# Kernel optimization log

Hardware: AMD Instinct MI355X
Metric: run time of the kernel (lower is better)

The kernel has to match this reference:

```python
import jax, jax.numpy as jnp
import numpy as np

S_IN, S_OUT = 64, 128
NX, NS, CIN, COUT = 40000, 200000, 128, 64


def _unique_coords(key, n, S):
    lin = jax.random.permutation(key, S ** 3)[:n]
    return jnp.stack([lin // (S * S), (lin // S) % S, lin % S], axis=-1).astype(jnp.int32)


def setup_inputs() -> dict:
    key = jax.random.key(0)
    ks = jax.random.split(key, 8)
    cords = _unique_coords(ks[0], NX, S_IN)          # unique low-res coords
    skip_cords = _unique_coords(ks[1], NS, S_OUT)    # unique high-res coords
    x_feats = jax.random.normal(ks[2], (NX, CIN), jnp.float32)
    skip_feats = jax.random.normal(ks[3], (NS, COUT), jnp.float32)
    w_up = jax.random.normal(ks[4], (8, CIN, COUT), jnp.float32) * 0.05
    w1 = jax.random.normal(ks[5], (27, COUT, COUT), jnp.float32) * 0.05
    w2 = jax.random.normal(ks[6], (27, COUT, COUT), jnp.float32) * 0.05
    w3 = jax.random.normal(ks[7], (27, COUT, COUT), jnp.float32) * 0.05
    ones = jnp.ones((COUT,), jnp.float32)
    zeros = jnp.zeros((COUT,), jnp.float32)
    return dict(x_feats=x_feats, skip_feats=skip_feats, w_up=w_up, w1=w1, w2=w2, w3=w3,
                g1=ones, b1=zeros, g2=ones, b2=zeros, g3=ones, b3=zeros,
                cords=cords, skip_cords=skip_cords, spatial_size=64)


def _lin(c, S):
    return (c[..., 0] * S + c[..., 1]) * S + c[..., 2]


def _bn(f, g, b):
    # BatchNorm1d, batch stats (track_running_stats=False), eps=1e-4, biased var
    mu = f.mean(axis=0)
    var = f.var(axis=0)
    return (f - mu) * jax.lax.rsqrt(var + 1e-4) * g + b


def _lrelu(z, s):
    return jnp.where(z >= 0, z, s * z)


def reference(x_feats, skip_feats, w_up, w1, w2, w3, g1, b1, g2, b2, g3, b3,
              cords, skip_cords, spatial_size):
    S = 2 * int(spatial_size)  # output spatial size after upsample
    Cout = w_up.shape[-1]
    # --- upsample: each active voxel c emits a 2x2x2 block at 2c+o, weight W[1-o] ---
    offs8 = jnp.stack(jnp.meshgrid(*([jnp.arange(2)] * 3), indexing='ij'), -1).reshape(8, 3).astype(jnp.int32)
    out_cords = ((2 * cords)[:, None, :] + offs8[None, :, :]).reshape(-1, 3)        # [8N,3]
    feats = jnp.einsum('nc,ocd->nod', x_feats, w_up[::-1]).reshape(-1, Cout)         # [8N,C]
    M = feats.shape[0]
    lin_out = _lin(out_cords, S)
    # --- sparse_add: hash-match skip coords, add matched skip features ---
    table_s = jnp.full((S ** 3,), -1, jnp.int32).at[_lin(skip_cords, S)].set(
        jnp.arange(skip_cords.shape[0], dtype=jnp.int32))
    j = table_s[lin_out]
    feats = feats + jnp.where((j >= 0)[:, None], skip_feats[jnp.clip(j, 0)], 0.0)
    # --- neighbor table for 3x3x3 submanifold convs over the fixed active set ---
    table_o = jnp.full((S ** 3,), -1, jnp.int32).at[lin_out].set(jnp.arange(M, dtype=jnp.int32))
    offs27 = jnp.stack(jnp.meshgrid(*([jnp.arange(-1, 2)] * 3), indexing='ij'), -1).reshape(27, 3).astype(jnp.int32)
    nb = out_cords[None, :, :] + offs27[:, None, :]                                  # [27,M,3]
    valid = jnp.all((nb >= 0) & (nb < S), axis=-1)
    lin_nb = jnp.where(valid, _lin(nb, S), 0)
    nbr = jnp.where(valid, table_o[lin_nb], -1)                                      # [27,M]

    def subconv(f, W):
        acc = jnp.zeros((M, W.shape[-1]), f.dtype)
        for k in range(27):  # fixed small kernel loop
            idx = nbr[k]
            m = (idx >= 0).astype(f.dtype)[:, None]
            acc = acc + (f[jnp.clip(idx, 0)] * m) @ W[k]
        return acc

    x1 = _lrelu(_bn(subconv(feats, w1), g1, b1), 0.05)
    x2 = _lrelu(_bn(subconv(x1, w2), g2, b2), 0.05)
    x3 = _bn(subconv(x2, w3), g3, b3)
    return _lrelu(x3 + x1, 0.333)
```

## Files before the change

kernel.cpp:

```cpp
#include <hip/hip_runtime.h>


#define S2 128
#define TABN (S2 * S2 * S2)

typedef __attribute__((ext_vector_type(8))) short short8;
typedef __attribute__((ext_vector_type(4))) float f32x4;

__device__ inline float b2f(unsigned short u) {
    return __uint_as_float(((unsigned)u) << 16);
}
__device__ inline unsigned short f2b(float f) {
    unsigned u = __float_as_uint(f);
    return (unsigned short)((u + 0x7FFF + ((u >> 16) & 1)) >> 16);
}

__global__ void k_scatter_skip(const int* __restrict__ sc, int* __restrict__ table_s, int NS) {
    int i = blockIdx.x * 256 + threadIdx.x;
    if (i >= NS) return;
    table_s[(sc[i * 3] * S2 + sc[i * 3 + 1]) * S2 + sc[i * 3 + 2]] = i;
}

__global__ void k_packw(const float* __restrict__ w, unsigned short* __restrict__ wpk) {
    int t = blockIdx.x * 256 + threadIdx.x;
    if (t >= 27 * 4096) return;
    int j = t & 7, l = (t >> 3) & 63, nt = (t >> 9) & 3, ks = (t >> 11) & 1, k = t >> 12;
    int d = ks * 32 + (l >> 4) * 8 + j;
    int c = nt * 16 + (l & 15);
    wpk[t] = f2b(w[(k * 64 + d) * 64 + c]);
}

__global__ __launch_bounds__(256) void k_upsample(
    const float* __restrict__ x, const float* __restrict__ wup,
    const int* __restrict__ cords, const float* __restrict__ skipf,
    const int* __restrict__ table_s, int* __restrict__ table_o,
    unsigned short* __restrict__ feats, int NX) {
    __shared__ float xl[16][132];
    int tid = threadIdx.x;
    int P0 = blockIdx.x * 16;
    {
        int p = tid >> 4, d0 = (tid & 15) * 8;
        const float* src = x + (size_t)(P0 + p) * 128 + d0;
        float4 a = *(const float4*)src;
        float4 b = *(const float4*)(src + 4);
        xl[p][d0 + 0] = a.x; xl[p][d0 + 1] = a.y; xl[p][d0 + 2] = a.z; xl[p][d0 + 3] = a.w;
        xl[p][d0 + 4] = b.x; xl[p][d0 + 5] = b.y; xl[p][d0 + 6] = b.z; xl[p][d0 + 7] = b.w;
    }
    __syncthreads();
    int c = tid & 63, g = tid >> 6;
    float acc[8][4];
#pragma unroll
    for (int o = 0; o < 8; ++o)
#pragma unroll
        for (int p = 0; p < 4; ++p) acc[o][p] = 0.f;
    for (int d = 0; d < 128; ++d) {
        float xv0 = xl[g * 4 + 0][d], xv1 = xl[g * 4 + 1][d];
        float xv2 = xl[g * 4 + 2][d], xv3 = xl[g * 4 + 3][d];
#pragma unroll
        for (int o = 0; o < 8; ++o) {
            float wv = wup[(size_t)(7 - o) * 8192 + d * 64 + c];
            acc[o][0] += xv0 * wv; acc[o][1] += xv1 * wv;
            acc[o][2] += xv2 * wv; acc[o][3] += xv3 * wv;
        }
    }
    for (int p = 0; p < 4; ++p) {
        int parent = P0 + g * 4 + p;
        int cx = cords[parent * 3], cy = cords[parent * 3 + 1], cz = cords[parent * 3 + 2];
#pragma unroll
        for (int o = 0; o < 8; ++o) {
            int X = 2 * cx + (o >> 2), Y = 2 * cy + ((o >> 1) & 1), Z = 2 * cz + (o & 1);
            int lin = (X * S2 + Y) * S2 + Z;
            int m = parent * 8 + o;
            int j = table_s[lin];
            float v = acc[o][p];
            if (j >= 0) v += skipf[(size_t)j * 64 + c];
            feats[(size_t)m * 64 + c] = f2b(v);
            if (c == 0) table_o[lin] = m;
        }
    }
}

__global__ void k_build_nbr(const int* __restrict__ cords, const int* __restrict__ table_o,
                            int* __restrict__ nbr, int M) {
    int m = blockIdx.x * 256 + threadIdx.x;
    if (m >= M) return;
    int n = m >> 3, o = m & 7;
    int X = 2 * cords[n * 3] + (o >> 2);
    int Y = 2 * cords[n * 3 + 1] + ((o >> 1) & 1);
    int Z = 2 * cords[n * 3 + 2] + (o & 1);
#pragma unroll
    for (int kk = 0; kk < 27; ++kk) {
        int nx = X + kk / 9 - 1, ny = Y + (kk / 3) % 3 - 1, nz = Z + kk % 3 - 1;
        int idx = -1;
        if ((unsigned)nx < (unsigned)S2 && (unsigned)ny < (unsigned)S2 && (unsigned)nz < (unsigned)S2)
            idx = table_o[(nx * S2 + ny) * S2 + nz];
        nbr[(size_t)kk * M + m] = idx;
    }
}

__global__ __launch_bounds__(256) void k_conv_mfma(
    const unsigned short* __restrict__ fin, const unsigned short* __restrict__ wpk,
    const int* __restrict__ nbr, unsigned short* __restrict__ zout,
    float* __restrict__ stats, int M) {
    int tid = threadIdx.x;
    int lane = tid & 63, wv = tid >> 6;
    int l15 = lane & 15, kg = lane >> 4;
    int rbase = blockIdx.x * 128 + wv * 32;

    f32x4 acc[2][4];
#pragma unroll
    for (int m = 0; m < 2; ++m)
#pragma unroll
        for (int nt = 0; nt < 4; ++nt) acc[m][nt] = (f32x4){0.f, 0.f, 0.f, 0.f};

    const short8 kzero = {0, 0, 0, 0, 0, 0, 0, 0};
    for (int k = 0; k < 27; ++k) {
        const int* nrow = nbr + (size_t)k * M + rbase;
        int i0 = nrow[l15];
        int i1 = nrow[16 + l15];
        const unsigned short* p0 = fin + (size_t)(i0 < 0 ? 0 : i0) * 64 + kg * 8;
        const unsigned short* p1 = fin + (size_t)(i1 < 0 ? 0 : i1) * 64 + kg * 8;
        short8 a00 = *(const short8*)p0;
        short8 a01 = *(const short8*)(p0 + 32);
        short8 a10 = *(const short8*)p1;
        short8 a11 = *(const short8*)(p1 + 32);
        if (i0 < 0) { a00 = kzero; a01 = kzero; }
        if (i1 < 0) { a10 = kzero; a11 = kzero; }
        const unsigned short* wb = wpk + (size_t)k * 4096 + lane * 8;
#pragma unroll
        for (int nt = 0; nt < 4; ++nt) {
            short8 b0 = *(const short8*)(wb + nt * 512);
            short8 b1 = *(const short8*)(wb + 2048 + nt * 512);
            acc[0][nt] = __builtin_amdgcn_mfma_f32_16x16x32_bf16(a00, b0, acc[0][nt], 0, 0, 0);
            acc[0][nt] = __builtin_amdgcn_mfma_f32_16x16x32_bf16(a01, b1, acc[0][nt], 0, 0, 0);
            acc[1][nt] = __builtin_amdgcn_mfma_f32_16x16x32_bf16(a10, b0, acc[1][nt], 0, 0, 0);
            acc[1][nt] = __builtin_amdgcn_mfma_f32_16x16x32_bf16(a11, b1, acc[1][nt], 0, 0, 0);
        }
    }

    float s[4] = {0.f, 0.f, 0.f, 0.f}, q[4] = {0.f, 0.f, 0.f, 0.f};
#pragma unroll
    for (int m = 0; m < 2; ++m)
#pragma unroll
        for (int nt = 0; nt < 4; ++nt)
#pragma unroll
            for (int j = 0; j < 4; ++j) {
                float v = acc[m][nt][j];
                int row = rbase + m * 16 + kg * 4 + j;
                zout[(size_t)row * 64 + nt * 16 + l15] = f2b(v);
                s[nt] += v; q[nt] += v * v;
            }
#pragma unroll
    for (int nt = 0; nt < 4; ++nt) {
        float ss = s[nt], qq = q[nt];
        ss += __shfl_xor(ss, 16); ss += __shfl_xor(ss, 32);
        qq += __shfl_xor(qq, 16); qq += __shfl_xor(qq, 32);
        if (kg == 0) {
            atomicAdd(&stats[nt * 16 + l15], ss);
            atomicAdd(&stats[64 + nt * 16 + l15], qq);
        }
    }
}

__global__ void k_finalize(const float* __restrict__ stats, const float* __restrict__ g,
                           const float* __restrict__ b, float* __restrict__ coef, float invM) {
    int c = threadIdx.x;
    if (c >= 64) return;
    float mu = stats[c] * invM;
    float var = stats[64 + c] * invM - mu * mu;
    float sc = g[c] * rsqrtf(var + 1e-4f);
    coef[c] = sc;
    coef[64 + c] = b[c] - mu * sc;
}

__global__ void k_xform(unsigned short* __restrict__ z, const float* __restrict__ coef, int n8) {
    int t = blockIdx.x * 256 + threadIdx.x;
    if (t >= n8) return;
    short8 v = ((const short8*)z)[t];
    int cb = (t * 8) & 63;
    short8 r;
#pragma unroll
    for (int j = 0; j < 8; ++j) {
        float f = b2f((unsigned short)v[j]) * coef[cb + j] + coef[64 + cb + j];
        f = fmaxf(f, 0.05f * f);
        r[j] = (short)f2b(f);
    }
    ((short8*)z)[t] = r;
}

__global__ void k_final(const unsigned short* __restrict__ z3,
                        const unsigned short* __restrict__ x1,
                        const float* __restrict__ coef3, float* __restrict__ out, int n8) {
    int t = blockIdx.x * 256 + threadIdx.x;
    if (t >= n8) return;
    short8 v3 = ((const short8*)z3)[t];
    short8 v1 = ((const short8*)x1)[t];
    int cb = (t * 8) & 63;
    float4 o0, o1;
    float rr[8];
#pragma unroll
    for (int j = 0; j < 8; ++j) {
        float f3 = b2f((unsigned short)v3[j]) * coef3[cb + j] + coef3[64 + cb + j];
        float r = f3 + b2f((unsigned short)v1[j]);
        rr[j] = fmaxf(r, 0.333f * r);
    }
    o0 = make_float4(rr[0], rr[1], rr[2], rr[3]);
    o1 = make_float4(rr[4], rr[5], rr[6], rr[7]);
    ((float4*)out)[t * 2] = o0;
    ((float4*)out)[t * 2 + 1] = o1;
}

extern "C" void kernel_launch(void* const* d_in, const int* in_sizes, int n_in,
                              void* d_out, int out_size, void* d_ws, size_t ws_size,
                              hipStream_t stream) {
    const float* x_feats    = (const float*)d_in[0];
    const float* skip_feats = (const float*)d_in[1];
    const float* w_up       = (const float*)d_in[2];
    const float* w1         = (const float*)d_in[3];
    const float* w2         = (const float*)d_in[4];
    const float* w3         = (const float*)d_in[5];
    const float* g1 = (const float*)d_in[6],  *b1 = (const float*)d_in[7];
    const float* g2 = (const float*)d_in[8],  *b2 = (const float*)d_in[9];
    const float* g3 = (const float*)d_in[10], *b3 = (const float*)d_in[11];
    const int* cords      = (const int*)d_in[12];
    const int* skip_cords = (const int*)d_in[13];
    int NX = in_sizes[12] / 3;
    int NS = in_sizes[13] / 3;
    int M = NX * 8;

    char* ws = (char*)d_ws;
    size_t off = 0;
    auto alloc = [&](size_t bytes) -> char* {
        char* p = ws + off;
        off += (bytes + 255) & ~(size_t)255;
        return p;
    };
    int* table_s = (int*)alloc((size_t)TABN * 4);
    int* table_o = (int*)alloc((size_t)TABN * 4);
    int* nbr     = (int*)alloc((size_t)27 * M * 4);
    unsigned short* A = (unsigned short*)alloc((size_t)M * 64 * 2);
    unsigned short* B = (unsigned short*)alloc((size_t)M * 64 * 2);
    unsigned short* C = (unsigned short*)alloc((size_t)M * 64 * 2);
    unsigned short* wp1 = (unsigned short*)alloc(27 * 4096 * 2);
    unsigned short* wp2 = (unsigned short*)alloc(27 * 4096 * 2);
    unsigned short* wp3 = (unsigned short*)alloc(27 * 4096 * 2);
    float* stats = (float*)alloc(384 * 4);
    float* coefs = (float*)alloc(384 * 4);

    hipMemsetAsync(table_s, 0xFF, (size_t)TABN * 4, stream);
    hipMemsetAsync(table_o, 0xFF, (size_t)TABN * 4, stream);
    hipMemsetAsync(stats, 0, 384 * 4, stream);

    float invM = 1.f / (float)M;
    int n8 = M * 64 / 8;

    k_scatter_skip<<<(NS + 255) / 256, 256, 0, stream>>>(skip_cords, table_s, NS);
    k_packw<<<432, 256, 0, stream>>>(w1, wp1);
    k_packw<<<432, 256, 0, stream>>>(w2, wp2);
    k_packw<<<432, 256, 0, stream>>>(w3, wp3);
    k_upsample<<<NX / 16, 256, 0, stream>>>(x_feats, w_up, cords, skip_feats,
                                            table_s, table_o, A, NX);
    k_build_nbr<<<(M + 255) / 256, 256, 0, stream>>>(cords, table_o, nbr, M);

    k_conv_mfma<<<M / 128, 256, 0, stream>>>(A, wp1, nbr, B, stats, M);
    k_finalize<<<1, 64, 0, stream>>>(stats, g1, b1, coefs, invM);
    k_xform<<<(n8 + 255) / 256, 256, 0, stream>>>(B, coefs, n8);

    k_conv_mfma<<<M / 128, 256, 0, stream>>>(B, wp2, nbr, C, stats + 128, M);
    k_finalize<<<1, 64, 0, stream>>>(stats + 128, g2, b2, coefs + 128, invM);
    k_xform<<<(n8 + 255) / 256, 256, 0, stream>>>(C, coefs + 128, n8);

    k_conv_mfma<<<M / 128, 256, 0, stream>>>(C, wp3, nbr, A, stats + 256, M);
    k_finalize<<<1, 64, 0, stream>>>(stats + 256, g3, b3, coefs + 256, invM);

    k_final<<<(n8 + 255) / 256, 256, 0, stream>>>(A, B, coefs + 256, (float*)d_out, n8);
}
```

Baseline: 1.370 ms.

## Restructure sparse conv: double-buffered gathers, 64-row waves, zero-row sentinel

The submanifold conv kernel now handles 256 rows per block (64 per wave) and stages the 27 neighbor-index rows into LDS up front. It double-buffers the gathered A fragments and weight fragments across kernel offsets so loads for offset k+1 are issued before the MFMAs for offset k. Missing neighbors now point to an extra zeroed sentinel row instead of using per-load masking. The aim is to hide gather latency and reuse each weight fragment over more rows, at the cost of higher register pressure (launch bounds 256,2) and half as many blocks.

Measured after the change: 1.105 ms. 19.4% less time.

```diff
diff --git a/kernel.cpp b/kernel.cpp
--- a/kernel.cpp
+++ b/kernel.cpp
@@ -94,59 +94,83 @@
         int idx = -1;
         if ((unsigned)nx < (unsigned)S2 && (unsigned)ny < (unsigned)S2 && (unsigned)nz < (unsigned)S2)
             idx = table_o[(nx * S2 + ny) * S2 + nz];
-        nbr[(size_t)kk * M + m] = idx;
-    }
-}
-
-__global__ __launch_bounds__(256) void k_conv_mfma(
+        nbr[(size_t)kk * M + m] = (idx < 0) ? M : idx;
+    }
+}
+
+__global__ __launch_bounds__(256, 2) void k_conv_mfma(
     const unsigned short* __restrict__ fin, const unsigned short* __restrict__ wpk,
     const int* __restrict__ nbr, unsigned short* __restrict__ zout,
     float* __restrict__ stats, int M) {
+    __shared__ int idx_lds[27 * 256];
     int tid = threadIdx.x;
     int lane = tid & 63, wv = tid >> 6;
     int l15 = lane & 15, kg = lane >> 4;
-    int rbase = blockIdx.x * 128 + wv * 32;
-
-    f32x4 acc[2][4];
-#pragma unroll
-    for (int m = 0; m < 2; ++m)
+    int rblk = blockIdx.x * 256;
+    int rw = wv * 64;
+
+    {
+        int col = (tid & 63) * 4;
+        for (int q = tid >> 6; q < 27; q += 4) {
+            int4 v = *(const int4*)(nbr + (size_t)q * M + rblk + col);
+            *(int4*)&idx_lds[q * 256 + col] = v;
+        }
+    }
+    __syncthreads();
+
+    f32x4 acc[4][4];
+#pragma unroll
+    for (int m = 0; m < 4; ++m)
 #pragma unroll
         for (int nt = 0; nt < 4; ++nt) acc[m][nt] = (f32x4){0.f, 0.f, 0.f, 0.f};
 
-    const short8 kzero = {0, 0, 0, 0, 0, 0, 0, 0};
-    for (int k = 0; k < 27; ++k) {
-        const int* nrow = nbr + (size_t)k * M + rbase;
-        int i0 = nrow[l15];
-        int i1 = nrow[16 + l15];
-        const unsigned short* p0 = fin + (size_t)(i0 < 0 ? 0 : i0) * 64 + kg * 8;
-        const unsigned short* p1 = fin + (size_t)(i1 < 0 ? 0 : i1) * 64 + kg * 8;
-        short8 a00 = *(const short8*)p0;
-        short8 a01 = *(const short8*)(p0 + 32);
-        short8 a10 = *(const short8*)p1;
-        short8 a11 = *(const short8*)(p1 + 32);
-        if (i0 < 0) { a00 = kzero; a01 = kzero; }
-        if (i1 < 0) { a10 = kzero; a11 = kzero; }
+    short8 A0[4][2], A1[4][2], B0[8], B1[8];
+
+    auto loadA = [&](short8 A[4][2], int k) {
+#pragma unroll
+        for (int m = 0; m < 4; ++m) {
+            int idx = idx_lds[k * 256 + rw + m * 16 + l15];
+            const unsigned short* p = fin + (size_t)idx * 64 + kg * 8;
+            A[m][0] = *(const short8*)p;
+            A[m][1] = *(const short8*)(p + 32);
+        }
+    };
+    auto loadB = [&](short8 B[8], int k) {
         const unsigned short* wb = wpk + (size_t)k * 4096 + lane * 8;
 #pragma unroll
-        for (int nt = 0; nt < 4; ++nt) {
-            short8 b0 = *(const short8*)(wb + nt * 512);
-            short8 b1 = *(const short8*)(wb + 2048 + nt * 512);
-            acc[0][nt] = __builtin_amdgcn_mfma_f32_16x16x32_bf16(a00, b0, acc[0][nt], 0, 0, 0);
-            acc[0][nt] = __builtin_amdgcn_mfma_f32_16x16x32_bf16(a01, b1, acc[0][nt], 0, 0, 0);
-            acc[1][nt] = __builtin_amdgcn_mfma_f32_16x16x32_bf16(a10, b0, acc[1][nt], 0, 0, 0);
-            acc[1][nt] = __builtin_amdgcn_mfma_f32_16x16x32_bf16(a11, b1, acc[1][nt], 0, 0, 0);
-        }
-    }
+        for (int ks = 0; ks < 2; ++ks)
+#pragma unroll
+            for (int nt = 0; nt < 4; ++nt)
+                B[ks * 4 + nt] = *(const short8*)(wb + ks * 2048 + nt * 512);
+    };
+    auto domfma = [&](short8 A[4][2], short8 B[8]) {
+#pragma unroll
+        for (int m = 0; m < 4; ++m)
+#pragma unroll
+            for (int nt = 0; nt < 4; ++nt) {
+                acc[m][nt] = __builtin_amdgcn_mfma_f32_16x16x32_bf16(A[m][0], B[nt], acc[m][nt], 0, 0, 0);
+                acc[m][nt] = __builtin_amdgcn_mfma_f32_16x16x32_bf16(A[m][1], B[4 + nt], acc[m][nt], 0, 0, 0);
+            }
+    };
+
+    loadA(A0, 0); loadB(B0, 0);
+    for (int k = 0; k < 26; k += 2) {
+        loadA(A1, k + 1); loadB(B1, k + 1);
+        domfma(A0, B0);
+        loadA(A0, k + 2); loadB(B0, k + 2);
+        domfma(A1, B1);
+    }
+    domfma(A0, B0);
 
     float s[4] = {0.f, 0.f, 0.f, 0.f}, q[4] = {0.f, 0.f, 0.f, 0.f};
 #pragma unroll
-    for (int m = 0; m < 2; ++m)
+    for (int m = 0; m < 4; ++m)
 #pragma unroll
         for (int nt = 0; nt < 4; ++nt)
 #pragma unroll
             for (int j = 0; j < 4; ++j) {
                 float v = acc[m][nt][j];
-                int row = rbase + m * 16 + kg * 4 + j;
+                int row = rblk + rw + m * 16 + kg * 4 + j;
                 zout[(size_t)row * 64 + nt * 16 + l15] = f2b(v);
                 s[nt] += v; q[nt] += v * v;
             }
@@ -196,7 +220,6 @@
     short8 v3 = ((const short8*)z3)[t];
     short8 v1 = ((const short8*)x1)[t];
     int cb = (t * 8) & 63;
-    float4 o0, o1;
     float rr[8];
 #pragma unroll
     for (int j = 0; j < 8; ++j) {
@@ -204,10 +227,8 @@
         float r = f3 + b2f((unsigned short)v1[j]);
         rr[j] = fmaxf(r, 0.333f * r);
     }
-    o0 = make_float4(rr[0], rr[1], rr[2], rr[3]);
-    o1 = make_float4(rr[4], rr[5], rr[6], rr[7]);
-    ((float4*)out)[t * 2] = o0;
-    ((float4*)out)[t * 2 + 1] = o1;
+    ((float4*)out)[t * 2] = make_float4(rr[0], rr[1], rr[2], rr[3]);
+    ((float4*)out)[t * 2 + 1] = make_float4(rr[4], rr[5], rr[6], rr[7]);
 }
 
 extern "C" void kernel_launch(void* const* d_in, const int* in_sizes, int n_in,
@@ -238,9 +259,9 @@
     int* table_s = (int*)alloc((size_t)TABN * 4);
     int* table_o = (int*)alloc((size_t)TABN * 4);
     int* nbr     = (int*)alloc((size_t)27 * M * 4);
-    unsigned short* A = (unsigned short*)alloc((size_t)M * 64 * 2);
-    unsigned short* B = (unsigned short*)alloc((size_t)M * 64 * 2);
-    unsigned short* C = (unsigned short*)alloc((size_t)M * 64 * 2);
+    unsigned short* A = (unsigned short*)alloc((size_t)(M + 1) * 64 * 2);
+    unsigned short* B = (unsigned short*)alloc((size_t)(M + 1) * 64 * 2);
+    unsigned short* C = (unsigned short*)alloc((size_t)(M + 1) * 64 * 2);
     unsigned short* wp1 = (unsigned short*)alloc(27 * 4096 * 2);
     unsigned short* wp2 = (unsigned short*)alloc(27 * 4096 * 2);
     unsigned short* wp3 = (unsigned short*)alloc(27 * 4096 * 2);
@@ -250,6 +271,9 @@
     hipMemsetAsync(table_s, 0xFF, (size_t)TABN * 4, stream);
     hipMemsetAsync(table_o, 0xFF, (size_t)TABN * 4, stream);
     hipMemsetAsync(stats, 0, 384 * 4, stream);
+    hipMemsetAsync(A + (size_t)M * 64, 0, 128, stream);
+    hipMemsetAsync(B + (size_t)M * 64, 0, 128, stream);
+    hipMemsetAsync(C + (size_t)M * 64, 0, 128, stream);
 
     float invM = 1.f / (float)M;
     int n8 = M * 64 / 8;
@@ -262,15 +286,15 @@
                                             table_s, table_o, A, NX);
     k_build_nbr<<<(M + 255) / 256, 256, 0, stream>>>(cords, table_o, nbr, M);
 
-    k_conv_mfma<<<M / 128, 256, 0, stream>>>(A, wp1, nbr, B, stats, M);
+    k_conv_mfma<<<M / 256, 256, 0, stream>>>(A, wp1, nbr, B, stats, M);
     k_finalize<<<1, 64, 0, stream>>>(stats, g1, b1, coefs, invM);
     k_xform<<<(n8 + 255) / 256, 256, 0, stream>>>(B, coefs, n8);
 
-    k_conv_mfma<<<M / 128, 256, 0, stream>>>(B, wp2, nbr, C, stats + 128, M);
+    k_conv_mfma<<<M / 256, 256, 0, stream>>>(B, wp2, nbr, C, stats + 128, M);
     k_finalize<<<1, 64, 0, stream>>>(stats + 128, g2, b2, coefs + 128, invM);
     k_xform<<<(n8 + 255) / 256, 256, 0, stream>>>(C, coefs + 128, n8);
 
-    k_conv_mfma<<<M / 128, 256, 0, stream>>>(C, wp3, nbr, A, stats + 256, M);
+    k_conv_mfma<<<M / 256, 256, 0, stream>>>(C, wp3, nbr, A, stats + 256, M);
     k_finalize<<<1, 64, 0, stream>>>(stats + 256, g3, b3, coefs + 256, invM);
 
     k_final<<<(n8 + 255) / 256, 256, 0, stream>>>(A, B, coefs + 256, (float*)d_out, n8);
```
